# Performance work log

Measured on AMD Instinct MI355X. Metric: run time of the kernel, lower is better.

The kernel has to match this reference:

```python
import jax, jax.numpy as jnp
import numpy as np
from jax import lax

B, N, C, W, D = 128, 16384, 8, 10, 3   # batch, input_size, n_channels, out_window, poly_degree
L = N - W + 1                          # in-filter tap length
EPS = 1e-5


def setup_inputs() -> dict:
    key = jax.random.key(0)
    ks = jax.random.split(key, 8)
    x = jax.random.normal(ks[0], (B, N, C, 2), dtype=jnp.float32)
    # torch Linear-style scale ~ 1/sqrt(fan_in)
    w_in_real = jax.random.normal(ks[1], (C, L), dtype=jnp.float32) * (L ** -0.5)
    w_in_imag = jax.random.normal(ks[2], (C, L), dtype=jnp.float32) * (L ** -0.5)
    fan_coeff = 2 * (C - 1) * D
    w_coeff = jax.random.normal(ks[3], (C, 2, fan_coeff), dtype=jnp.float32) * (fan_coeff ** -0.5)
    w_out_real = jax.random.normal(ks[4], (C, W), dtype=jnp.float32) * (W ** -0.5)
    w_out_imag = jax.random.normal(ks[5], (C, W), dtype=jnp.float32) * (W ** -0.5)
    bn_gamma = jnp.ones((C,), dtype=jnp.float32)
    bn_beta = jnp.zeros((C,), dtype=jnp.float32)
    return {"x": x, "w_in_real": w_in_real, "w_in_imag": w_in_imag,
            "w_coeff": w_coeff, "w_out_real": w_out_real,
            "w_out_imag": w_out_imag, "bn_gamma": bn_gamma, "bn_beta": bn_beta}


# complement index map: row c lists all channels != c
_IDX = np.array([[j for j in range(C) if j != c] for c in range(C)])  # (C, C-1)


def _grouped_fir(sig, w):
    # sig: (B, N, C); per-channel length-L correlation -> (B, W, C)
    out = lax.conv_general_dilated(
        jnp.transpose(sig, (0, 2, 1)),      # (B, C, N)
        w[:, None, :],                      # (C, 1, L)
        window_strides=(1,), padding='VALID', feature_group_count=C)
    return jnp.transpose(out, (0, 2, 1))    # (B, W, C)


def reference(x, w_in_real, w_in_imag, w_coeff, w_out_real, w_out_imag, bn_gamma, bn_beta):
    fr = _grouped_fir(x[..., 0], w_in_real)   # (B, W, C)
    fi = _grouped_fir(x[..., 1], w_in_imag)   # (B, W, C)

    # polynomial expansion: pow_d = fr^d + fi^d, d = 1..D
    powd = jnp.stack([fr ** d + fi ** d for d in range(1, D + 1)], axis=-1)  # (B, W, C, D)
    poly_r = powd * fr[..., None]
    poly_i = powd * fi[..., None]

    # cross-channel coeff layers: input layout = [real(all j != c), imag(all j != c)]
    rg = poly_r[:, :, _IDX, :]                      # (B, W, C, C-1, D)
    ig = poly_i[:, :, _IDX, :]
    Wc = w_coeff.reshape(C, 2, 2, C - 1, D)         # (c, out, real/imag half, j, d)
    nonlin = (jnp.einsum('bwcjd,cpjd->bwcp', rg, Wc[:, :, 0]) +
              jnp.einsum('bwcjd,cpjd->bwcp', ig, Wc[:, :, 1]))  # (B, W, C, 2)

    out_r = jnp.einsum('bwc,cw->bc', nonlin[..., 0], w_out_real)
    out_i = jnp.einsum('bwc,cw->bc', nonlin[..., 1], w_out_imag)
    out = jnp.stack([out_r, out_i], axis=-1)        # (B, C, 2)

    # BatchNorm1d over (batch, last) per channel, training-mode batch stats
    mean = out.mean(axis=(0, 2), keepdims=True)
    var = out.var(axis=(0, 2), keepdims=True)
    return (out - mean) / jnp.sqrt(var + EPS) * bn_gamma[None, :, None] + bn_beta[None, :, None]
```

## Files before the change

### kernel.cpp

```cpp
#include <hip/hip_runtime.h>

#define BB 128
#define NN 16384
#define CC 8
#define WW 10
#define LL 16375
#define NT 512
#define NTILES (NN / NT)
#define BT 8
#define BTILES (BB / BT)
#define WSL (NT + 9)
#define BPB 16
#define ABLK (BB / BPB)

typedef float f2_t __attribute__((ext_vector_type(2)));

__global__ __launch_bounds__(256) void k_fir(const float* __restrict__ x,
                                             const float* __restrict__ wr,
                                             const float* __restrict__ wi,
                                             float* __restrict__ fpart) {
  __shared__ float smem[WSL * CC * 2];
  f2_t* sw2 = (f2_t*)smem;

  int nt = blockIdx.x & (NTILES - 1);
  int bt = blockIdx.x >> 5;
  int tid = threadIdx.x;
  int ntile = nt * NT;
  int l0 = ntile - 9;

  {
    int cs = tid >> 5;
    int jj = tid & 31;
    for (int j = jj; j < WSL; j += 32) {
      int l = l0 + j;
      float a = 0.f, bb = 0.f;
      if (l >= 0 && l < LL) { a = wr[cs * LL + l]; bb = wi[cs * LL + l]; }
      f2_t v; v[0] = a; v[1] = bb;
      sw2[cs * WSL + j] = v;
    }
  }
  __syncthreads();

  int c    = tid & 7;
  int bsub = (tid >> 3) & 7;
  int nh   = tid >> 6;
  int b    = bt * BT + bsub;

  const f2_t* __restrict__ xp = ((const f2_t*)x) + ((size_t)b * NN + ntile + nh * 128) * CC + c;
  const f2_t* wp = sw2 + c * WSL + nh * 128 + 9;

  f2_t acc[WW];
#pragma unroll
  for (int w = 0; w < WW; ++w) acc[w] = (f2_t)0.f;

  f2_t prev[9];
#pragma unroll
  for (int k = 0; k < 9; ++k) prev[k] = wp[k - 9];

  for (int g = 0; g < 8; ++g) {
    f2_t wv[16], xv[16];
#pragma unroll
    for (int u = 0; u < 16; ++u) {
      wv[u] = wp[g * 16 + u];
      xv[u] = xp[(size_t)(g * 16 + u) * CC];
    }
#pragma unroll
    for (int u = 0; u < 16; ++u) {
#pragma unroll
      for (int w = 0; w < WW; ++w) {
        int idx = u - w;
        f2_t wt = (idx >= 0) ? wv[idx] : prev[idx + 9];
        acc[w][0] += xv[u][0] * wt[0];
        acc[w][1] += xv[u][1] * wt[1];
      }
    }
#pragma unroll
    for (int k = 0; k < 9; ++k) prev[k] = wv[7 + k];
  }

  __syncthreads();
  float* red = smem;
  int rb = (nh * 8 + bsub) * 160 + c * 2;
#pragma unroll
  for (int w = 0; w < WW; ++w) {
    red[rb + w * 16]     = acc[w][0];
    red[rb + w * 16 + 1] = acc[w][1];
  }
  __syncthreads();
  for (int t = tid; t < BT * 160; t += 256) {
    int bs = t / 160;
    int r  = t - bs * 160;
    float s = red[(0 * 8 + bs) * 160 + r] + red[(1 * 8 + bs) * 160 + r]
            + red[(2 * 8 + bs) * 160 + r] + red[(3 * 8 + bs) * 160 + r];
    fpart[((size_t)(bt * BT + bs) * NTILES + nt) * 160 + r] = s;
  }
}

__global__ __launch_bounds__(256) void k_nonlin(const float* __restrict__ fpart,
                                                const float* __restrict__ wc,
                                                const float* __restrict__ wor,
                                                const float* __restrict__ woi,
                                                float* __restrict__ oraw,
                                                float* __restrict__ part) {
  __shared__ float sred[BPB][164];
  __shared__ float swc[704];
  __shared__ float swout[160];

  int tid = threadIdx.x;
  int blk = blockIdx.x;
  int b0 = blk * BPB;

  for (int i = tid; i < 672; i += 256) swc[i] = wc[i];
  if (tid < 80) swout[tid] = wor[tid];
  else if (tid < 160) swout[tid] = woi[tid - 80];

  {
    const float4* fp4 = (const float4*)fpart;
    for (int o4 = tid; o4 < BPB * 40; o4 += 256) {
      int bl = o4 / 40;
      int r4 = o4 - bl * 40;
      float4 s = {0.f, 0.f, 0.f, 0.f};
      size_t base = ((size_t)(b0 + bl) * NTILES) * 40 + r4;
#pragma unroll
      for (int seg = 0; seg < NTILES; ++seg) {
        float4 v = fp4[base + (size_t)seg * 40];
        s.x += v.x; s.y += v.y; s.z += v.z; s.w += v.w;
      }
      int r = r4 * 4;
      sred[bl][r] = s.x; sred[bl][r + 1] = s.y; sred[bl][r + 2] = s.z; sred[bl][r + 3] = s.w;
    }
  }
  __syncthreads();

  int b = tid >> 4;
  int c = (tid >> 1) & 7;
  int p = tid & 1;

  float wreg[8][2][3];
#pragma unroll
  for (int j = 0; j < 8; ++j) {
    int jj = j - (j > c ? 1 : 0);
    if (j == c) jj = 0;
#pragma unroll
    for (int ri = 0; ri < 2; ++ri)
#pragma unroll
      for (int d = 0; d < 3; ++d) {
        float v = swc[(c * 2 + p) * 42 + ri * 21 + jj * 3 + d];
        wreg[j][ri][d] = (j == c) ? 0.f : v;
      }
  }

  float o = 0.f;
  const float* wop = swout + p * 80 + c * 10;
#pragma unroll
  for (int w = 0; w < WW; ++w) {
    float4 f0 = *(const float4*)&sred[b][w * 16];
    float4 f1 = *(const float4*)&sred[b][w * 16 + 4];
    float4 f2 = *(const float4*)&sred[b][w * 16 + 8];
    float4 f3 = *(const float4*)&sred[b][w * 16 + 12];
    float fv[16] = {f0.x, f0.y, f0.z, f0.w, f1.x, f1.y, f1.z, f1.w,
                    f2.x, f2.y, f2.z, f2.w, f3.x, f3.y, f3.z, f3.w};
    float nl0 = 0.f, nl1 = 0.f, nl2 = 0.f;
#pragma unroll
    for (int j = 0; j < 8; ++j) {
      float r  = fv[2 * j];
      float im = fv[2 * j + 1];
      float r2 = r * r, i2 = im * im;
      float pw0 = r + im;
      float pw1 = r2 + i2;
      float pw2 = r2 * r + i2 * im;
      nl0 += (pw0 * r) * wreg[j][0][0] + (pw0 * im) * wreg[j][1][0];
      nl1 += (pw1 * r) * wreg[j][0][1] + (pw1 * im) * wreg[j][1][1];
      nl2 += (pw2 * r) * wreg[j][0][2] + (pw2 * im) * wreg[j][1][2];
    }
    o += (nl0 + nl1 + nl2) * wop[w];
  }

  oraw[((size_t)(b0 + b) * CC + c) * 2 + p] = o;

  __shared__ float sval[256], ssq[256];
  sval[tid] = o;
  ssq[tid]  = o * o;
  __syncthreads();
  if (tid < 8) {
    float S = 0.f, Q = 0.f;
#pragma unroll
    for (int k = 0; k < 32; ++k) {
      int t = (k >> 1) * 16 + tid * 2 + (k & 1);
      S += sval[t];
      Q += ssq[t];
    }
    part[(blk * 8 + tid) * 2 + 0] = S;
    part[(blk * 8 + tid) * 2 + 1] = Q;
  }
}

__global__ __launch_bounds__(256) void k_bn(const float* __restrict__ oraw,
                                            const float* __restrict__ part,
                                            const float* __restrict__ gamma,
                                            const float* __restrict__ beta,
                                            float* __restrict__ out) {
  __shared__ float mv[8], iv[8], bv[8];
  int tid = threadIdx.x;
  if (tid < 8) {
    float S = 0.f, Q = 0.f;
#pragma unroll
    for (int blk = 0; blk < ABLK; ++blk) {
      S += part[(blk * 8 + tid) * 2 + 0];
      Q += part[(blk * 8 + tid) * 2 + 1];
    }
    float mean = S * (1.0f / 256.0f);
    float var  = Q * (1.0f / 256.0f) - mean * mean;
    mv[tid] = mean;
    iv[tid] = gamma[tid] * rsqrtf(var + 1e-5f);
    bv[tid] = beta[tid];
  }
  __syncthreads();
  for (int i = tid; i < BB * CC * 2; i += 256) {
    int c = (i >> 1) & 7;
    out[i] = (oraw[i] - mv[c]) * iv[c] + bv[c];
  }
}

extern "C" void kernel_launch(void* const* d_in, const int* in_sizes, int n_in,
                              void* d_out, int out_size, void* d_ws, size_t ws_size,
                              hipStream_t stream) {
  const float* x   = (const float*)d_in[0];
  const float* wr  = (const float*)d_in[1];
  const float* wi  = (const float*)d_in[2];
  const float* wc  = (const float*)d_in[3];
  const float* wor = (const float*)d_in[4];
  const float* woi = (const float*)d_in[5];
  const float* gm  = (const float*)d_in[6];
  const float* bt  = (const float*)d_in[7];
  float* out = (float*)d_out;

  float* ws    = (float*)d_ws;
  float* fpart = ws;
  float* oraw  = fpart + (size_t)BB * NTILES * 160;
  float* part  = oraw + BB * CC * 2;

  k_fir<<<dim3(BTILES * NTILES), dim3(256), 0, stream>>>(x, wr, wi, fpart);
  k_nonlin<<<dim3(ABLK), dim3(256), 0, stream>>>(fpart, wc, wor, woi, oraw, part);
  k_bn<<<dim3(1), dim3(256), 0, stream>>>(oraw, part, gm, bt, out);
}
```

Measured before the change: 46.20 us.

## Restructure FIR kernel to float4 channel-pair loads with wave-shuffle reduction

Each thread in the FIR kernel now handles two channels at once using 16-byte float4 loads of x and of interleaved weights, instead of 8-byte float2. The batch tile shrinks to 4, so the grid doubles. Each thread covers a 32-sample slice of the 512 tile instead of 128, using a rolling 16-entry weight window. Partial sums are first reduced across lanes with xor shuffles, then across waves through shared memory. The aim is fewer, wider memory transactions and cheaper reductions, at the cost of more blocks each redundantly reloading the weight tile.

```diff
diff --git a/kernel.cpp b/kernel.cpp
--- a/kernel.cpp
+++ b/kernel.cpp
@@ -7,20 +7,20 @@
 #define LL 16375
 #define NT 512
 #define NTILES (NN / NT)
-#define BT 8
+#define BT 4
 #define BTILES (BB / BT)
 #define WSL (NT + 9)
 #define BPB 16
 #define ABLK (BB / BPB)
 
-typedef float f2_t __attribute__((ext_vector_type(2)));
+typedef float f4_t __attribute__((ext_vector_type(4)));
 
 __global__ __launch_bounds__(256) void k_fir(const float* __restrict__ x,
                                              const float* __restrict__ wr,
                                              const float* __restrict__ wi,
                                              float* __restrict__ fpart) {
-  __shared__ float smem[WSL * CC * 2];
-  f2_t* sw2 = (f2_t*)smem;
+  __shared__ float smem[WSL * 16 + 16];
+  f4_t* sw = (f4_t*)smem;
 
   int nt = blockIdx.x & (NTILES - 1);
   int bt = blockIdx.x >> 5;
@@ -29,69 +29,85 @@
   int l0 = ntile - 9;
 
   {
-    int cs = tid >> 5;
-    int jj = tid & 31;
-    for (int j = jj; j < WSL; j += 32) {
+    int c2s = tid >> 6;
+    int ca = 2 * c2s, cb = 2 * c2s + 1;
+    for (int j = tid & 63; j < WSL; j += 64) {
       int l = l0 + j;
-      float a = 0.f, bb = 0.f;
-      if (l >= 0 && l < LL) { a = wr[cs * LL + l]; bb = wi[cs * LL + l]; }
-      f2_t v; v[0] = a; v[1] = bb;
-      sw2[cs * WSL + j] = v;
-    }
-  }
-  __syncthreads();
-
-  int c    = tid & 7;
-  int bsub = (tid >> 3) & 7;
-  int nh   = tid >> 6;
+      f4_t v = (f4_t)0.f;
+      if (l >= 0 && l < LL) {
+        v[0] = wr[(size_t)ca * LL + l];
+        v[1] = wi[(size_t)ca * LL + l];
+        v[2] = wr[(size_t)cb * LL + l];
+        v[3] = wi[(size_t)cb * LL + l];
+      }
+      sw[j * 4 + c2s] = v;
+    }
+  }
+  __syncthreads();
+
+  int c2   = tid & 3;
+  int bsub = (tid >> 2) & 3;
+  int nh   = tid >> 4;
   int b    = bt * BT + bsub;
-
-  const f2_t* __restrict__ xp = ((const f2_t*)x) + ((size_t)b * NN + ntile + nh * 128) * CC + c;
-  const f2_t* wp = sw2 + c * WSL + nh * 128 + 9;
-
-  f2_t acc[WW];
-#pragma unroll
-  for (int w = 0; w < WW; ++w) acc[w] = (f2_t)0.f;
-
-  f2_t prev[9];
-#pragma unroll
-  for (int k = 0; k < 9; ++k) prev[k] = wp[k - 9];
-
-  for (int g = 0; g < 8; ++g) {
-    f2_t wv[16], xv[16];
+  int n0   = ntile + nh * 32;
+
+  const f4_t* __restrict__ xp = ((const f4_t*)x) + ((size_t)b * NN + n0) * 4 + c2;
+  const f4_t* swp = sw + (nh * 32 + 9) * 4 + c2;
+
+  f4_t acc[WW];
+#pragma unroll
+  for (int w = 0; w < WW; ++w) acc[w] = (f4_t)0.f;
+
+  f4_t wv[16];
+#pragma unroll
+  for (int k = 0; k < 9; ++k) wv[7 + k] = swp[4 * (k - 9)];
+
+#pragma unroll
+  for (int g = 0; g < 2; ++g) {
+#pragma unroll
+    for (int j = 0; j < 7; ++j) wv[j] = swp[4 * (16 * g + j)];
 #pragma unroll
     for (int u = 0; u < 16; ++u) {
-      wv[u] = wp[g * 16 + u];
-      xv[u] = xp[(size_t)(g * 16 + u) * CC];
-    }
-#pragma unroll
-    for (int u = 0; u < 16; ++u) {
+      f4_t xv = xp[(size_t)(16 * g + u) * 4];
 #pragma unroll
       for (int w = 0; w < WW; ++w) {
-        int idx = u - w;
-        f2_t wt = (idx >= 0) ? wv[idx] : prev[idx + 9];
-        acc[w][0] += xv[u][0] * wt[0];
-        acc[w][1] += xv[u][1] * wt[1];
-      }
-    }
-#pragma unroll
-    for (int k = 0; k < 9; ++k) prev[k] = wv[7 + k];
-  }
-
-  __syncthreads();
-  float* red = smem;
-  int rb = (nh * 8 + bsub) * 160 + c * 2;
-#pragma unroll
-  for (int w = 0; w < WW; ++w) {
-    red[rb + w * 16]     = acc[w][0];
-    red[rb + w * 16 + 1] = acc[w][1];
+        f4_t wt = wv[(u - w + 16) & 15];
+        acc[w][0] += xv[0] * wt[0];
+        acc[w][1] += xv[1] * wt[1];
+        acc[w][2] += xv[2] * wt[2];
+        acc[w][3] += xv[3] * wt[3];
+      }
+      if (u <= 8) wv[u + 7] = swp[4 * (16 * g + u + 7)];
+    }
+  }
+
+#pragma unroll
+  for (int w = 0; w < WW; ++w)
+#pragma unroll
+    for (int e = 0; e < 4; ++e) {
+      acc[w][e] += __shfl_xor(acc[w][e], 16);
+      acc[w][e] += __shfl_xor(acc[w][e], 32);
+    }
+
+  __syncthreads();
+  int wave = tid >> 6, lane = tid & 63;
+  if (lane < 16) {
+#pragma unroll
+    for (int w = 0; w < WW; ++w)
+      *(f4_t*)&smem[(wave * 16 + lane) * 40 + w * 4] = acc[w];
   }
   __syncthreads();
   for (int t = tid; t < BT * 160; t += 256) {
     int bs = t / 160;
     int r  = t - bs * 160;
-    float s = red[(0 * 8 + bs) * 160 + r] + red[(1 * 8 + bs) * 160 + r]
-            + red[(2 * 8 + bs) * 160 + r] + red[(3 * 8 + bs) * 160 + r];
+    int w  = r >> 4;
+    int cc = (r >> 1) & 7;
+    int ri = r & 1;
+    int ln = (cc >> 1) + 4 * bs;
+    int e  = (cc & 1) * 2 + ri;
+    float s = 0.f;
+#pragma unroll
+    for (int wv_ = 0; wv_ < 4; ++wv_) s += smem[(wv_ * 16 + ln) * 40 + w * 4 + e];
     fpart[((size_t)(bt * BT + bs) * NTILES + nt) * 160 + r] = s;
   }
 }
```

Result: no change. 45.52 us (-1.5%).
